# Kernel optimization log

Hardware: AMD Instinct MI355X
Metric: run time of the kernel (lower is better)

Reference implementation:

```python
import jax, jax.numpy as jnp
import numpy as np

N_NODES = 100000
N_EDGES = 1600000
N_GRAPHS = 128
DIM = 128
N_LAYERS = 4
EPS = 1e-5


def setup_inputs() -> dict:
    key = jax.random.key(0)
    ks = jax.random.split(key, 8)
    h = jax.random.normal(ks[0], (N_NODES, DIM), dtype=jnp.float32)
    src = jax.random.randint(ks[1], (N_EDGES,), 0, N_NODES, dtype=jnp.int32)
    dst = jax.random.randint(ks[2], (N_EDGES,), 0, N_NODES, dtype=jnp.int32)
    graph_id = jnp.sort(jax.random.randint(ks[3], (N_NODES,), 0, N_GRAPHS, dtype=jnp.int32))
    sc = 1.0 / np.sqrt(DIM)
    W_embed = jax.random.normal(ks[4], (DIM, DIM), dtype=jnp.float32) * sc
    b_embed = jnp.zeros((DIM,), jnp.float32)
    W_layers = jax.random.normal(ks[5], (N_LAYERS, DIM, DIM), dtype=jnp.float32) * sc
    b_layers = jnp.zeros((N_LAYERS, DIM), jnp.float32)
    gamma = jnp.ones((N_LAYERS, DIM), jnp.float32)
    beta = jnp.zeros((N_LAYERS, DIM), jnp.float32)
    return {"h": h, "src": src, "dst": dst, "graph_id": graph_id,
            "W_embed": W_embed, "b_embed": b_embed, "W_layers": W_layers,
            "b_layers": b_layers, "gamma": gamma, "beta": beta}


def _gcn_forward(h, src, dst, graph_id, W_embed, b_embed, W_layers, b_layers, gamma, beta):
    # symmetric GraphConv normalization (norm='both'): D_out^{-1/2} on src, D_in^{-1/2} on dst
    ones_e = jnp.ones((src.shape[0],), h.dtype)
    deg_out = jax.ops.segment_sum(ones_e, src, num_segments=N_NODES)
    deg_in = jax.ops.segment_sum(ones_e, dst, num_segments=N_NODES)
    norm_src = jax.lax.rsqrt(jnp.maximum(deg_out, 1.0))
    norm_dst = jax.lax.rsqrt(jnp.maximum(deg_in, 1.0))

    # input embedding (dropout = identity in eval)
    h = h @ W_embed + b_embed

    for l in range(N_LAYERS):
        h_in = h
        # gather-aggregate-scatter: m_e = h_src * norm_src; sum into dst; scale by norm_dst
        m = (h * norm_src[:, None])[src]                         # [E, D]
        agg = jax.ops.segment_sum(m, dst, num_segments=N_NODES)  # [N, D]
        hl = (agg * norm_dst[:, None]) @ W_layers[l] + b_layers[l]
        # batch norm over node dimension (training-mode batch stats)
        mu = jnp.mean(hl, axis=0)
        var = jnp.var(hl, axis=0)
        hl = (hl - mu) * jax.lax.rsqrt(var + EPS) * gamma[l] + beta[l]
        hl = jax.nn.relu(hl)
        h = hl + h_in  # residual (dims match all layers)

    # mean readout per graph
    sums = jax.ops.segment_sum(h, graph_id, num_segments=N_GRAPHS)           # [G, D]
    cnts = jax.ops.segment_sum(jnp.ones((N_NODES,), h.dtype), graph_id, num_segments=N_GRAPHS)
    return sums / jnp.maximum(cnts, 1.0)[:, None]


def reference(h, src, dst, graph_id, W_embed, b_embed, W_layers, b_layers, gamma, beta):
    return _gcn_forward(h, src, dst, graph_id, W_embed, b_embed, W_layers, b_layers, gamma, beta)
```

## Files before the change

kernel.cpp:

```cpp
#include <hip/hip_runtime.h>
#include <hip/hip_bf16.h>
#include <hip/hip_fp16.h>


#define N_NODES 100000
#define N_EDGES 1600000
#define N_GRAPHS 128
#define DIM 128
#define N_LAYERS 4
#define BN_EPS 1e-5f
#define NBUCK 196
#define EPB 6250
#define SREP 64

typedef __attribute__((ext_vector_type(8))) _Float16 half8;
typedef __attribute__((ext_vector_type(4))) float floatx4;
typedef __attribute__((ext_vector_type(2))) float floatx2;

__global__ __launch_bounds__(256) void binA_k(const int* __restrict__ src,
                                              const int* __restrict__ dst,
                                              int* __restrict__ cnt_d,
                                              int* __restrict__ cnt_s,
                                              int* __restrict__ bh_d,
                                              int* __restrict__ bh_s) {
  __shared__ int hd[NBUCK], hs[NBUCK];
  int t = threadIdx.x;
  for (int i = t; i < NBUCK; i += 256) { hd[i] = 0; hs[i] = 0; }
  __syncthreads();
  int e0 = blockIdx.x * EPB;
  for (int e = e0 + t; e < e0 + EPB; e += 256) {
    atomicAdd(&hd[dst[e] >> 9], 1);
    atomicAdd(&hs[src[e] >> 9], 1);
  }
  __syncthreads();
  for (int i = t; i < NBUCK; i += 256) {
    int v = hd[i], v2 = hs[i];
    bh_d[blockIdx.x * NBUCK + i] = v;
    bh_s[blockIdx.x * NBUCK + i] = v2;
    if (v) atomicAdd(&cnt_d[i], v);
    if (v2) atomicAdd(&cnt_s[i], v2);
  }
}

__global__ __launch_bounds__(256) void scan196_k(
    const int* __restrict__ cnt_d, const int* __restrict__ cnt_s,
    int* __restrict__ base_d, int* __restrict__ cur_d,
    int* __restrict__ base_s, int* __restrict__ cur_s,
    int* __restrict__ row_start) {
  __shared__ int sd[256], ss[256];
  int t = threadIdx.x;
  int vd = (t < NBUCK) ? cnt_d[t] : 0;
  int vs = (t < NBUCK) ? cnt_s[t] : 0;
  sd[t] = vd;
  ss[t] = vs;
  __syncthreads();
  for (int off = 1; off < 256; off <<= 1) {
    int ad = (t >= off) ? sd[t - off] : 0;
    int as = (t >= off) ? ss[t - off] : 0;
    __syncthreads();
    sd[t] += ad;
    ss[t] += as;
    __syncthreads();
  }
  if (t < NBUCK) {
    base_d[t] = sd[t] - vd;
    cur_d[t] = sd[t] - vd;
    base_s[t] = ss[t] - vs;
    cur_s[t] = ss[t] - vs;
  }
  if (t == 0) {
    base_d[NBUCK] = N_EDGES;
    base_s[NBUCK] = N_EDGES;
    row_start[N_NODES] = N_EDGES;
  }
}

__global__ __launch_bounds__(256) void scat_k(
    const int* __restrict__ src, const int* __restrict__ dst,
    int* __restrict__ cur_d, int* __restrict__ cur_s,
    const int* __restrict__ bh_d, const int* __restrict__ bh_s,
    int* __restrict__ packed, unsigned short* __restrict__ locs) {
  __shared__ int hd[NBUCK], hs[NBUCK];
  int t = threadIdx.x;
  for (int i = t; i < NBUCK; i += 256) {
    hd[i] = bh_d[blockIdx.x * NBUCK + i];
    hs[i] = bh_s[blockIdx.x * NBUCK + i];
  }
  __syncthreads();
  if (t < NBUCK) {
    hd[t] = atomicAdd(&cur_d[t], hd[t]);
    hs[t] = atomicAdd(&cur_s[t], hs[t]);
  }
  __syncthreads();
  int e0 = blockIdx.x * EPB;
  for (int e = e0 + t; e < e0 + EPB; e += 256) {
    int s = src[e], d = dst[e];
    int slot = atomicAdd(&hd[d >> 9], 1);
    packed[slot] = ((d & 511) << 17) | s;
    int slot2 = atomicAdd(&hs[s >> 9], 1);
    locs[slot2] = (unsigned short)(s & 511);
  }
}

__global__ __launch_bounds__(256) void cdcs_k(
    const int* __restrict__ base_d, const int* __restrict__ packed,
    int* __restrict__ row_start, int* __restrict__ csr_src,
    float* __restrict__ norm_dst, const int* __restrict__ base_s,
    const unsigned short* __restrict__ locs, float* __restrict__ norm_src) {
  __shared__ int sdeg[512], sinc[512], scur[512];
  int t = threadIdx.x;
  if (blockIdx.x >= NBUCK) {
    int b = blockIdx.x - NBUCK;
    int nbase = b << 9;
    int e0 = base_s[b], e1 = base_s[b + 1];
    sdeg[t] = 0;
    sdeg[t + 256] = 0;
    __syncthreads();
    for (int e = e0 + t; e < e1; e += 256) atomicAdd(&sdeg[locs[e]], 1);
    __syncthreads();
#pragma unroll
    for (int half = 0; half < 2; ++half) {
      int j = t + half * 256;
      int node = nbase + j;
      if (node < N_NODES) {
        int d = sdeg[j];
        norm_src[node] = rsqrtf((float)(d > 1 ? d : 1));
      }
    }
    return;
  }
  int b = blockIdx.x;
  int nbase = b << 9;
  int e0 = base_d[b], e1 = base_d[b + 1];
  sdeg[t] = 0;
  sdeg[t + 256] = 0;
  __syncthreads();
  for (int e = e0 + t; e < e1; e += 256) atomicAdd(&sdeg[packed[e] >> 17], 1);
  __syncthreads();
  sinc[t] = sdeg[t];
  sinc[t + 256] = sdeg[t + 256];
  __syncthreads();
  for (int off = 1; off < 512; off <<= 1) {
    int a0 = (t >= off) ? sinc[t - off] : 0;
    int i1 = t + 256;
    int a1 = (i1 >= off) ? sinc[i1 - off] : 0;
    __syncthreads();
    sinc[t] += a0;
    sinc[i1] += a1;
    __syncthreads();
  }
#pragma unroll
  for (int half = 0; half < 2; ++half) {
    int j = t + half * 256;
    int lofs = e0 + sinc[j] - sdeg[j];
    scur[j] = lofs;
    int node = nbase + j;
    if (node < N_NODES) {
      row_start[node] = lofs;
      int d = sdeg[j];
      norm_dst[node] = rsqrtf((float)(d > 1 ? d : 1));
    }
  }
  __syncthreads();
  for (int e = e0 + t; e < e1; e += 256) {
    int p = packed[e];
    int slot = atomicAdd(&scur[p >> 17], 1);
    csr_src[slot] = p & 0x1FFFF;
  }
}

__global__ __launch_bounds__(256) void wswz_k(const float* __restrict__ W_embed,
                                              const float* __restrict__ W_layers,
                                              __half* __restrict__ Bsw) {
  int m = blockIdx.x >> 3, ct = blockIdx.x & 7;
  const float* Wm =
      (m == 0) ? W_embed : (W_layers + (size_t)(m - 1) * 16384);
  int ks = threadIdx.x >> 6, lane = threadIdx.x & 63;
  int n = ct * 16 + (lane & 15);
  int k0 = ks * 32 + (lane >> 4) * 8;
  __half* o = Bsw + ((((size_t)m * 8 + ct) * 4 + ks) * 64 + lane) * 8;
#pragma unroll
  for (int j = 0; j < 8; ++j) o[j] = __float2half(Wm[(k0 + j) * 128 + n]);
}

__device__ inline void mfma_core16(const __half* sA,
                                   const __half* __restrict__ Bsw,
                                   floatx4 (&acc)[8], int w, int lane,
                                   int quad, int lrow) {
#pragma unroll
  for (int ct = 0; ct < 8; ++ct) acc[ct] = (floatx4)(0.f);
#pragma unroll
  for (int ks = 0; ks < 4; ++ks) {
    int m = w * 16 + lrow;
    half8 afrag = *(const half8*)(&sA[m * 136 + ks * 32 + quad * 8]);
#pragma unroll
    for (int ct = 0; ct < 8; ++ct) {
      half8 bfrag = *(const half8*)(&Bsw[(((size_t)ct * 4 + ks) * 64 + lane) * 8]);
      acc[ct] = __builtin_amdgcn_mfma_f32_16x16x32_f16(afrag, bfrag, acc[ct],
                                                       0, 0, 0);
    }
  }
}

__device__ inline void accf8x8(float (&a)[8], uint2 v) {
  floatx2 f;
  f = __builtin_amdgcn_cvt_pk_f32_fp8(v.x, false); a[0] += f.x; a[1] += f.y;
  f = __builtin_amdgcn_cvt_pk_f32_fp8(v.x, true);  a[2] += f.x; a[3] += f.y;
  f = __builtin_amdgcn_cvt_pk_f32_fp8(v.y, false); a[4] += f.x; a[5] += f.y;
  f = __builtin_amdgcn_cvt_pk_f32_fp8(v.y, true);  a[6] += f.x; a[7] += f.y;
}

__global__ __launch_bounds__(256) void mfma_gemm_f32in(
    const float* __restrict__ X32, const __half* __restrict__ Bsw,
    const float* __restrict__ bias, __half* __restrict__ A16,
    unsigned char* __restrict__ S8, const float* __restrict__ norm_src) {
  __shared__ __half sA[64 * 136];
  const int tid = threadIdx.x;
  const int w = tid >> 6, lane = tid & 63;
  const int quad = lane >> 4, lrow = lane & 15;
  const int row_base = blockIdx.x * 64;

#pragma unroll
  for (int i = 0; i < 8; ++i) {
    int g = i * 256 + tid;
    int r = g >> 5, q = g & 31;
    int row = row_base + r;
    float4 v = make_float4(0.f, 0.f, 0.f, 0.f);
    if (row < N_NODES) v = ((const float4*)X32)[(size_t)row * 32 + q];
    union { __half2 h[2]; float f[2]; } u;
    u.h[0] = __floats2half2_rn(v.x, v.y);
    u.h[1] = __floats2half2_rn(v.z, v.w);
    *(float2*)(&sA[r * 136 + q * 4]) = *(float2*)u.f;
  }
  __syncthreads();

  floatx4 acc[8];
  mfma_core16(sA, Bsw, acc, w, lane, quad, lrow);

  float bcol[8];
#pragma unroll
  for (int ct = 0; ct < 8; ++ct) bcol[ct] = bias[ct * 16 + lrow];

  float* sC = (float*)sA;
#pragma unroll
  for (int h = 0; h < 2; ++h) {
    __syncthreads();
    if ((w >> 1) == h) {
      int hw = w & 1;
#pragma unroll
      for (int ct = 0; ct < 8; ++ct)
#pragma unroll
        for (int reg = 0; reg < 4; ++reg)
          sC[(hw * 16 + quad * 4 + reg) * 132 + ct * 16 + lrow] =
              acc[ct][reg] + bcol[ct];
    }
    __syncthreads();
#pragma unroll
    for (int k = 0; k < 4; ++k) {
      int c = k * 256 + tid;
      int hr = c >> 5;
      int col = (c & 31) * 4;
      int row = row_base + h * 32 + hr;
      if (row < N_NODES) {
        float4 y = *(const float4*)&sC[hr * 132 + col];
        union { __half2 hh[2]; float2 f; } u;
        u.hh[0] = __floats2half2_rn(y.x, y.y);
        u.hh[1] = __floats2half2_rn(y.z, y.w);
        *(float2*)(A16 + (size_t)row * 128 + col) = u.f;
        float ns = norm_src[row];
        unsigned pb = 0;
        pb = __builtin_amdgcn_cvt_pk_fp8_f32(y.x * ns, y.y * ns, pb, false);
        pb = __builtin_amdgcn_cvt_pk_fp8_f32(y.z * ns, y.w * ns, pb, true);
        *(unsigned*)(S8 + (size_t)row * 128 + col) = pb;
      }
    }
  }
}

__global__ __launch_bounds__(256, 8) void gather16_k(
    const uint2* __restrict__ Hs, const int* __restrict__ row_start,
    const int* __restrict__ csr_src, const float* __restrict__ norm_dst,
    __half* __restrict__ out) {
  int node = (blockIdx.x * 256 + threadIdx.x) >> 4;
  int l16 = threadIdx.x & 15;
  int l8 = l16 & 7;
  if (node >= N_NODES) return;
  int s0 = row_start[node], s1 = row_start[node + 1];
  float a[8];
#pragma unroll
  for (int i = 0; i < 8; ++i) a[i] = 0.f;
  int deg = s1 - s0;
  int nfull = deg >> 3;
  int e = s0;
  if (nfull) {
    int idx = csr_src[e + l8];
    for (int k = 0; k < nfull; ++k) {
      uint2 v0 = Hs[(size_t)__shfl(idx, 0, 16) * 16 + l16];
      uint2 v1 = Hs[(size_t)__shfl(idx, 1, 16) * 16 + l16];
      uint2 v2 = Hs[(size_t)__shfl(idx, 2, 16) * 16 + l16];
      uint2 v3 = Hs[(size_t)__shfl(idx, 3, 16) * 16 + l16];
      uint2 v4 = Hs[(size_t)__shfl(idx, 4, 16) * 16 + l16];
      uint2 v5 = Hs[(size_t)__shfl(idx, 5, 16) * 16 + l16];
      uint2 v6 = Hs[(size_t)__shfl(idx, 6, 16) * 16 + l16];
      uint2 v7 = Hs[(size_t)__shfl(idx, 7, 16) * 16 + l16];
      int pe = e + 8 + l8;
      int idx_n = csr_src[pe < N_EDGES ? pe : (N_EDGES - 1)];
      accf8x8(a, v0); accf8x8(a, v1); accf8x8(a, v2); accf8x8(a, v3);
      accf8x8(a, v4); accf8x8(a, v5); accf8x8(a, v6); accf8x8(a, v7);
      idx = idx_n;
      e += 8;
    }
  }
  int cnt = s1 - e;
  if (cnt) {
    int idx = (l8 < cnt) ? csr_src[e + l8] : 0;
    int j = 0;
    for (; j + 4 <= cnt; j += 4) {
      uint2 v0 = Hs[(size_t)__shfl(idx, j, 16) * 16 + l16];
      uint2 v1 = Hs[(size_t)__shfl(idx, j + 1, 16) * 16 + l16];
      uint2 v2 = Hs[(size_t)__shfl(idx, j + 2, 16) * 16 + l16];
      uint2 v3 = Hs[(size_t)__shfl(idx, j + 3, 16) * 16 + l16];
      accf8x8(a, v0); accf8x8(a, v1); accf8x8(a, v2); accf8x8(a, v3);
    }
    for (; j < cnt; ++j) {
      accf8x8(a, Hs[(size_t)__shfl(idx, j, 16) * 16 + l16]);
    }
  }
  float nd = norm_dst[node];
  union { __half2 hh[4]; float4 f; } u;
#pragma unroll
  for (int q = 0; q < 4; ++q)
    u.hh[q] = __floats2half2_rn(a[2 * q] * nd, a[2 * q + 1] * nd);
  *(float4*)(out + (size_t)node * 128 + l16 * 8) = u.f;
}

__global__ __launch_bounds__(256) void mfma_gemm_f16(
    const __half* __restrict__ X16, const __half* __restrict__ Bsw,
    const float* __restrict__ bias, __half* __restrict__ hl16,
    float* __restrict__ stats) {
  __shared__ __half sA[64 * 136];
  __shared__ float sred[1024];
  const int tid = threadIdx.x;
  const int w = tid >> 6, lane = tid & 63;
  const int quad = lane >> 4, lrow = lane & 15;
  const int row_base = blockIdx.x * 64;

#pragma unroll
  for (int i = 0; i < 4; ++i) {
    int g = i * 256 + tid;
    int r = g >> 4, p = g & 15;
    int row = row_base + r;
    float4 v = make_float4(0.f, 0.f, 0.f, 0.f);
    if (row < N_NODES) v = ((const float4*)X16)[(size_t)row * 16 + p];
    *(float4*)(&sA[r * 136 + p * 8]) = v;
  }
  __syncthreads();

  floatx4 acc[8];
  mfma_core16(sA, Bsw, acc, w, lane, quad, lrow);

  float bcol[8], psum[8], pqsum[8];
#pragma unroll
  for (int ct = 0; ct < 8; ++ct) {
    bcol[ct] = bias[ct * 16 + lrow];
    psum[ct] = 0.f;
    pqsum[ct] = 0.f;
#pragma unroll
    for (int reg = 0; reg < 4; ++reg) {
      int row = row_base + w * 16 + quad * 4 + reg;
      if (row < N_NODES) {
        float y = acc[ct][reg] + bcol[ct];
        psum[ct] += y;
        pqsum[ct] += y * y;
      }
    }
  }
#pragma unroll
  for (int ct = 0; ct < 8; ++ct) {
    psum[ct] += __shfl_xor(psum[ct], 16, 64);
    psum[ct] += __shfl_xor(psum[ct], 32, 64);
    pqsum[ct] += __shfl_xor(pqsum[ct], 16, 64);
    pqsum[ct] += __shfl_xor(pqsum[ct], 32, 64);
  }
  if (quad == 0) {
#pragma unroll
    for (int ct = 0; ct < 8; ++ct) {
      sred[w * 128 + ct * 16 + lrow] = psum[ct];
      sred[512 + w * 128 + ct * 16 + lrow] = pqsum[ct];
    }
  }
  __syncthreads();
  if (tid < 128) {
    float s = sred[tid] + sred[128 + tid] + sred[256 + tid] + sred[384 + tid];
    float q = sred[512 + tid] + sred[640 + tid] + sred[768 + tid] +
              sred[896 + tid];
    float* st = stats + (size_t)(blockIdx.x & (SREP - 1)) * 256;
    atomicAdd(&st[tid], s);
    atomicAdd(&st[128 + tid], q);
  }

  float* sC = (float*)sA;
#pragma unroll
  for (int h = 0; h < 2; ++h) {
    __syncthreads();
    if ((w >> 1) == h) {
      int hw = w & 1;
#pragma unroll
      for (int ct = 0; ct < 8; ++ct)
#pragma unroll
        for (int reg = 0; reg < 4; ++reg)
          sC[(hw * 16 + quad * 4 + reg) * 132 + ct * 16 + lrow] =
              acc[ct][reg] + bcol[ct];
    }
    __syncthreads();
#pragma unroll
    for (int k = 0; k < 4; ++k) {
      int c = k * 256 + tid;
      int hr = c >> 5;
      int col = (c & 31) * 4;
      int row = row_base + h * 32 + hr;
      if (row < N_NODES) {
        float4 y = *(const float4*)&sC[hr * 132 + col];
        union { __half2 hh[2]; float2 f; } u;
        u.hh[0] = __floats2half2_rn(y.x, y.y);
        u.hh[1] = __floats2half2_rn(y.z, y.w);
        *(float2*)(hl16 + (size_t)row * 128 + col) = u.f;
      }
    }
  }
}

__global__ __launch_bounds__(128) void bn_fin_k(const float* __restrict__ stats,
                                                const float* __restrict__ gamma,
                                                const float* __restrict__ beta,
                                                float* __restrict__ sc_sh) {
  int c = threadIdx.x;
  float s = 0.f, q = 0.f;
  for (int r = 0; r < SREP; ++r) {
    s += stats[r * 256 + c];
    q += stats[r * 256 + 128 + c];
  }
  const float invn = 1.0f / (float)N_NODES;
  float mean = s * invn;
  float var = q * invn - mean * mean;
  var = fmaxf(var, 0.f);
  float sc = gamma[c] * rsqrtf(var + BN_EPS);
  sc_sh[c] = sc;
  sc_sh[128 + c] = beta[c] - mean * sc;
}

__global__ __launch_bounds__(256) void bnrelu_k(
    const __half* __restrict__ hl16, __half* __restrict__ A16,
    unsigned char* __restrict__ S8, const float* __restrict__ sc_sh,
    const float* __restrict__ norm_src, int write_scaled) {
  int idx = blockIdx.x * 256 + threadIdx.x;
  int node = idx >> 4;
  int c8 = idx & 15;
  float4 hv4 = *(const float4*)(hl16 + (size_t)idx * 8);
  float4 av4 = *(const float4*)(A16 + (size_t)idx * 8);
  const __half2* hp = (const __half2*)&hv4;
  const __half2* ap = (const __half2*)&av4;
  const float4* sv = (const float4*)sc_sh;
  float4 s0 = sv[c8 * 2], s1 = sv[c8 * 2 + 1];
  float4 b0 = sv[32 + c8 * 2], b1 = sv[32 + c8 * 2 + 1];
  float n = write_scaled ? norm_src[node] : 0.f;
  float2 f0 = __half22float2(hp[0]), f1 = __half22float2(hp[1]);
  float2 f2 = __half22float2(hp[2]), f3 = __half22float2(hp[3]);
  float2 a0 = __half22float2(ap[0]), a1 = __half22float2(ap[1]);
  float2 a2 = __half22float2(ap[2]), a3 = __half22float2(ap[3]);
  float v[8];
  v[0] = fmaxf(f0.x * s0.x + b0.x, 0.f) + a0.x;
  v[1] = fmaxf(f0.y * s0.y + b0.y, 0.f) + a0.y;
  v[2] = fmaxf(f1.x * s0.z + b0.z, 0.f) + a1.x;
  v[3] = fmaxf(f1.y * s0.w + b0.w, 0.f) + a1.y;
  v[4] = fmaxf(f2.x * s1.x + b1.x, 0.f) + a2.x;
  v[5] = fmaxf(f2.y * s1.y + b1.y, 0.f) + a2.y;
  v[6] = fmaxf(f3.x * s1.z + b1.z, 0.f) + a3.x;
  v[7] = fmaxf(f3.y * s1.w + b1.w, 0.f) + a3.y;
  union { __half2 h[4]; float4 f; } ua;
#pragma unroll
  for (int q = 0; q < 4; ++q)
    ua.h[q] = __floats2half2_rn(v[2 * q], v[2 * q + 1]);
  *(float4*)(A16 + (size_t)idx * 8) = ua.f;
  if (write_scaled) {
    unsigned lo = 0, hi = 0;
    lo = __builtin_amdgcn_cvt_pk_fp8_f32(v[0] * n, v[1] * n, lo, false);
    lo = __builtin_amdgcn_cvt_pk_fp8_f32(v[2] * n, v[3] * n, lo, true);
    hi = __builtin_amdgcn_cvt_pk_fp8_f32(v[4] * n, v[5] * n, hi, false);
    hi = __builtin_amdgcn_cvt_pk_fp8_f32(v[6] * n, v[7] * n, hi, true);
    ((uint2*)S8)[idx] = make_uint2(lo, hi);
  }
}

__global__ __launch_bounds__(128) void gsum_k(const __half* __restrict__ A16,
                                              const int* __restrict__ gid,
                                              float* gsum) {
  int c = threadIdx.x;
  int n0 = blockIdx.x * 128;
  int n1 = n0 + 128;
  if (n1 > N_NODES) n1 = N_NODES;
  int cur = gid[n0];
  float local = 0.f;
  for (int n = n0; n < n1; ++n) {
    int g = gid[n];
    if (g != cur) {
      atomicAdd(&gsum[cur * 128 + c], local);
      local = 0.f;
      cur = g;
    }
    local += __half2float(A16[(size_t)n * 128 + c]);
  }
  atomicAdd(&gsum[cur * 128 + c], local);
}

__global__ __launch_bounds__(128) void gout_k(const float* __restrict__ gsum,
                                              const int* __restrict__ gid,
                                              float* __restrict__ out) {
  __shared__ int bnd[2];
  int g = blockIdx.x, c = threadIdx.x;
  if (c < 2) {
    int target = g + c;
    int lo = 0, hi = N_NODES;
    while (lo < hi) {
      int mid = (lo + hi) >> 1;
      if (gid[mid] < target) lo = mid + 1; else hi = mid;
    }
    bnd[c] = lo;
  }
  __syncthreads();
  float cnt = (float)(bnd[1] - bnd[0]);
  if (cnt < 1.f) cnt = 1.f;
  out[g * 128 + c] = gsum[g * 128 + c] / cnt;
}

extern "C" void kernel_launch(void* const* d_in, const int* in_sizes, int n_in,
                              void* d_out, int out_size, void* d_ws,
                              size_t ws_size, hipStream_t stream) {
  const float* h = (const float*)d_in[0];
  const int* src = (const int*)d_in[1];
  const int* dst = (const int*)d_in[2];
  const int* gid = (const int*)d_in[3];
  const float* W_embed = (const float*)d_in[4];
  const float* b_embed = (const float*)d_in[5];
  const float* W_layers = (const float*)d_in[6];
  const float* b_layers = (const float*)d_in[7];
  const float* gamma = (const float*)d_in[8];
  const float* beta = (const float*)d_in[9];
  float* out = (float*)d_out;
  (void)in_sizes; (void)n_in; (void)out_size; (void)ws_size;

  char* ws = (char*)d_ws;
  size_t o = 0;
  auto alloc = [&](size_t bytes) -> char* {
    char* p = ws + o;
    o = (o + bytes + 255) & ~(size_t)255;
    return p;
  };
  int* cnt_d = (int*)alloc(NBUCK * 4);
  int* cnt_s = (int*)alloc(NBUCK * 4);
  int* base_d = (int*)alloc((NBUCK + 1) * 4);
  int* cur_d = (int*)alloc(NBUCK * 4);
  int* base_s = (int*)alloc((NBUCK + 1) * 4);
  int* cur_s = (int*)alloc(NBUCK * 4);
  int* bh_d = (int*)alloc((size_t)256 * NBUCK * 4);
  int* bh_s = (int*)alloc((size_t)256 * NBUCK * 4);
  float* norm_src = (float*)alloc(N_NODES * 4);
  float* norm_dst = (float*)alloc(N_NODES * 4);
  int* row_start = (int*)alloc((N_NODES + 1) * 4);
  int* csr_src = (int*)alloc((size_t)N_EDGES * 4);
  int* packed = (int*)alloc((size_t)N_EDGES * 4);
  unsigned short* locs = (unsigned short*)alloc((size_t)N_EDGES * 2);
  float* stats4 = (float*)alloc((size_t)N_LAYERS * SREP * 256 * 4);
  float* gsum = (float*)alloc(N_GRAPHS * 128 * 4);
  float* sc_sh = (float*)alloc(256 * 4);
  __half* Bsw = (__half*)alloc(5 * 16384 * 2);
  __half* A16 = (__half*)alloc((size_t)N_NODES * 128 * 2);
  unsigned char* P0f8 = (unsigned char*)alloc((size_t)N_NODES * 128);
  __half* P1h = (__half*)alloc((size_t)N_NODES * 128 * 2);
  __half* H16 = (__half*)alloc((size_t)N_NODES * 128 * 2);

  hipMemsetAsync(cnt_d, 0, 2048, stream);
  hipMemsetAsync(stats4, 0, (size_t)N_LAYERS * SREP * 256 * 4 + 65536, stream);

  binA_k<<<256, 256, 0, stream>>>(src, dst, cnt_d, cnt_s, bh_d, bh_s);
  scan196_k<<<1, 256, 0, stream>>>(cnt_d, cnt_s, base_d, cur_d, base_s, cur_s,
                                   row_start);
  scat_k<<<256, 256, 0, stream>>>(src, dst, cur_d, cur_s, bh_d, bh_s, packed,
                                  locs);
  cdcs_k<<<2 * NBUCK, 256, 0, stream>>>(base_d, packed, row_start, csr_src,
                                        norm_dst, base_s, locs, norm_src);

  wswz_k<<<40, 256, 0, stream>>>(W_embed, W_layers, Bsw);

  mfma_gemm_f32in<<<(N_NODES + 63) / 64, 256, 0, stream>>>(
      h, Bsw, b_embed, A16, P0f8, norm_src);

  for (int l = 0; l < N_LAYERS; ++l) {
    float* stats = stats4 + (size_t)l * SREP * 256;
    gather16_k<<<(N_NODES * 16 + 255) / 256, 256, 0, stream>>>(
        (const uint2*)P0f8, row_start, csr_src, norm_dst, P1h);
    mfma_gemm_f16<<<(N_NODES + 63) / 64, 256, 0, stream>>>(
        P1h, Bsw + (size_t)(1 + l) * 16384, b_layers + l * DIM, H16, stats);
    bn_fin_k<<<1, 128, 0, stream>>>(stats, gamma + l * DIM, beta + l * DIM,
                                    sc_sh);
    bnrelu_k<<<(N_NODES * 16 + 255) / 256, 256, 0, stream>>>(
        H16, A16, P0f8, sc_sh, norm_src, (l < N_LAYERS - 1) ? 1 : 0);
  }

  gsum_k<<<(N_NODES + 127) / 128, 128, 0, stream>>>(A16, gid, gsum);
  gout_k<<<N_GRAPHS, 128, 0, stream>>>(gsum, gid, out);
}
```

Before: 505.0 us.

## Split fp8 gather source into column slabs and gather slab-by-slab per node

The fp8 scaled feature matrix is re-laid-out into four 32-column slabs of 3.2 MB each, written that way by the embed GEMM and the BN/ReLU kernel. The gather kernel now uses 4 lanes per node and loops over the slabs, so each pass randomly gathers from a smaller working set that can stay cache-resident. Loads use nontemporal hints. The cost is rereading the CSR indices four times, less thread parallelism per node, and a serialized slab loop.

Measured after the change: 906.7 us. 79.5% more time.

```diff
diff --git a/kernel.cpp b/kernel.cpp
--- a/kernel.cpp
+++ b/kernel.cpp
@@ -12,10 +12,20 @@
 #define NBUCK 196
 #define EPB 6250
 #define SREP 64
+#define SLABQ (N_NODES * 4)
 
 typedef __attribute__((ext_vector_type(8))) _Float16 half8;
 typedef __attribute__((ext_vector_type(4))) float floatx4;
 typedef __attribute__((ext_vector_type(2))) float floatx2;
+
+__device__ inline uint2 ntload_u2(const uint2* p) {
+  unsigned long long v =
+      __builtin_nontemporal_load((const unsigned long long*)p);
+  uint2 r;
+  r.x = (unsigned)v;
+  r.y = (unsigned)(v >> 32);
+  return r;
+}
 
 __global__ __launch_bounds__(256) void binA_k(const int* __restrict__ src,
                                               const int* __restrict__ dst,
@@ -271,67 +281,69 @@
         unsigned pb = 0;
         pb = __builtin_amdgcn_cvt_pk_fp8_f32(y.x * ns, y.y * ns, pb, false);
         pb = __builtin_amdgcn_cvt_pk_fp8_f32(y.z * ns, y.w * ns, pb, true);
-        *(unsigned*)(S8 + (size_t)row * 128 + col) = pb;
+        ((unsigned*)S8)[(size_t)(col >> 5) * (N_NODES * 8) + row * 8 +
+                        ((col & 31) >> 2)] = pb;
       }
     }
   }
 }
 
-__global__ __launch_bounds__(256, 8) void gather16_k(
+__global__ __launch_bounds__(256, 8) void gather4_k(
     const uint2* __restrict__ Hs, const int* __restrict__ row_start,
     const int* __restrict__ csr_src, const float* __restrict__ norm_dst,
     __half* __restrict__ out) {
-  int node = (blockIdx.x * 256 + threadIdx.x) >> 4;
-  int l16 = threadIdx.x & 15;
-  int l8 = l16 & 7;
+  int node = (blockIdx.x * 256 + threadIdx.x) >> 2;
+  int l4 = threadIdx.x & 3;
   if (node >= N_NODES) return;
   int s0 = row_start[node], s1 = row_start[node + 1];
-  float a[8];
-#pragma unroll
-  for (int i = 0; i < 8; ++i) a[i] = 0.f;
   int deg = s1 - s0;
   int nfull = deg >> 3;
-  int e = s0;
-  if (nfull) {
-    int idx = csr_src[e + l8];
-    for (int k = 0; k < nfull; ++k) {
-      uint2 v0 = Hs[(size_t)__shfl(idx, 0, 16) * 16 + l16];
-      uint2 v1 = Hs[(size_t)__shfl(idx, 1, 16) * 16 + l16];
-      uint2 v2 = Hs[(size_t)__shfl(idx, 2, 16) * 16 + l16];
-      uint2 v3 = Hs[(size_t)__shfl(idx, 3, 16) * 16 + l16];
-      uint2 v4 = Hs[(size_t)__shfl(idx, 4, 16) * 16 + l16];
-      uint2 v5 = Hs[(size_t)__shfl(idx, 5, 16) * 16 + l16];
-      uint2 v6 = Hs[(size_t)__shfl(idx, 6, 16) * 16 + l16];
-      uint2 v7 = Hs[(size_t)__shfl(idx, 7, 16) * 16 + l16];
-      int pe = e + 8 + l8;
-      int idx_n = csr_src[pe < N_EDGES ? pe : (N_EDGES - 1)];
-      accf8x8(a, v0); accf8x8(a, v1); accf8x8(a, v2); accf8x8(a, v3);
-      accf8x8(a, v4); accf8x8(a, v5); accf8x8(a, v6); accf8x8(a, v7);
-      idx = idx_n;
-      e += 8;
-    }
-  }
-  int cnt = s1 - e;
-  if (cnt) {
-    int idx = (l8 < cnt) ? csr_src[e + l8] : 0;
-    int j = 0;
-    for (; j + 4 <= cnt; j += 4) {
-      uint2 v0 = Hs[(size_t)__shfl(idx, j, 16) * 16 + l16];
-      uint2 v1 = Hs[(size_t)__shfl(idx, j + 1, 16) * 16 + l16];
-      uint2 v2 = Hs[(size_t)__shfl(idx, j + 2, 16) * 16 + l16];
-      uint2 v3 = Hs[(size_t)__shfl(idx, j + 3, 16) * 16 + l16];
-      accf8x8(a, v0); accf8x8(a, v1); accf8x8(a, v2); accf8x8(a, v3);
-    }
-    for (; j < cnt; ++j) {
-      accf8x8(a, Hs[(size_t)__shfl(idx, j, 16) * 16 + l16]);
-    }
-  }
   float nd = norm_dst[node];
-  union { __half2 hh[4]; float4 f; } u;
-#pragma unroll
-  for (int q = 0; q < 4; ++q)
-    u.hh[q] = __floats2half2_rn(a[2 * q] * nd, a[2 * q + 1] * nd);
-  *(float4*)(out + (size_t)node * 128 + l16 * 8) = u.f;
+#pragma unroll 1
+  for (int slab = 0; slab < 4; ++slab) {
+    const uint2* Hsl = Hs + (size_t)slab * SLABQ;
+    float a[8];
+#pragma unroll
+    for (int i = 0; i < 8; ++i) a[i] = 0.f;
+    int e = s0;
+    if (nfull) {
+      int idxA = csr_src[e + l4];
+      int idxB = csr_src[e + 4 + l4];
+      for (int k = 0; k < nfull; ++k) {
+        uint2 v0 = ntload_u2(&Hsl[(size_t)__shfl(idxA, 0, 4) * 4 + l4]);
+        uint2 v1 = ntload_u2(&Hsl[(size_t)__shfl(idxA, 1, 4) * 4 + l4]);
+        uint2 v2 = ntload_u2(&Hsl[(size_t)__shfl(idxA, 2, 4) * 4 + l4]);
+        uint2 v3 = ntload_u2(&Hsl[(size_t)__shfl(idxA, 3, 4) * 4 + l4]);
+        uint2 v4 = ntload_u2(&Hsl[(size_t)__shfl(idxB, 0, 4) * 4 + l4]);
+        uint2 v5 = ntload_u2(&Hsl[(size_t)__shfl(idxB, 1, 4) * 4 + l4]);
+        uint2 v6 = ntload_u2(&Hsl[(size_t)__shfl(idxB, 2, 4) * 4 + l4]);
+        uint2 v7 = ntload_u2(&Hsl[(size_t)__shfl(idxB, 3, 4) * 4 + l4]);
+        int pa = e + 8 + l4, pb = e + 12 + l4;
+        int idxA_n = csr_src[pa < N_EDGES ? pa : (N_EDGES - 1)];
+        int idxB_n = csr_src[pb < N_EDGES ? pb : (N_EDGES - 1)];
+        accf8x8(a, v0); accf8x8(a, v1); accf8x8(a, v2); accf8x8(a, v3);
+        accf8x8(a, v4); accf8x8(a, v5); accf8x8(a, v6); accf8x8(a, v7);
+        idxA = idxA_n;
+        idxB = idxB_n;
+        e += 8;
+      }
+    }
+    int cnt = s1 - e;
+    if (cnt) {
+      int iA = (l4 < cnt) ? csr_src[e + l4] : 0;
+      int iB = (4 + l4 < cnt) ? csr_src[e + 4 + l4] : 0;
+      int jm = cnt < 4 ? cnt : 4;
+      for (int j = 0; j < jm; ++j)
+        accf8x8(a, ntload_u2(&Hsl[(size_t)__shfl(iA, j, 4) * 4 + l4]));
+      for (int j = 4; j < cnt; ++j)
+        accf8x8(a, ntload_u2(&Hsl[(size_t)__shfl(iB, j - 4, 4) * 4 + l4]));
+    }
+    union { __half2 hh[4]; float4 f; } u;
+#pragma unroll
+    for (int q = 0; q < 4; ++q)
+      u.hh[q] = __floats2half2_rn(a[2 * q] * nd, a[2 * q + 1] * nd);
+    *(float4*)(out + (size_t)node * 128 + slab * 32 + l4 * 8) = u.f;
+  }
 }
 
 __global__ __launch_bounds__(256) void mfma_gemm_f16(
@@ -488,7 +500,8 @@
     lo = __builtin_amdgcn_cvt_pk_fp8_f32(v[2] * n, v[3] * n, lo, true);
     hi = __builtin_amdgcn_cvt_pk_fp8_f32(v[4] * n, v[5] * n, hi, false);
     hi = __builtin_amdgcn_cvt_pk_fp8_f32(v[6] * n, v[7] * n, hi, true);
-    ((uint2*)S8)[idx] = make_uint2(lo, hi);
+    ((uint2*)S8)[(size_t)(c8 >> 2) * SLABQ + node * 4 + (c8 & 3)] =
+        make_uint2(lo, hi);
   }
 }
 
@@ -597,7 +610,7 @@
 
   for (int l = 0; l < N_LAYERS; ++l) {
     float* stats = stats4 + (size_t)l * SREP * 256;
-    gather16_k<<<(N_NODES * 16 + 255) / 256, 256, 0, stream>>>(
+    gather4_k<<<(N_NODES * 4 + 255) / 256, 256, 0, stream>>>(
         (const uint2*)P0f8, row_start, csr_src, norm_dst, P1h);
     mfma_gemm_f16<<<(N_NODES + 63) / 64, 256, 0, stream>>>(
         P1h, Bsw + (size_t)(1 + l) * 16384, b_layers + l * DIM, H16, stats);
```
